# Kernel optimization log

Measured on AMD Instinct MI355X. Metric: run time of the kernel, lower is better.

Reference implementation:

```python
import jax, jax.numpy as jnp
import numpy as np

B, T, C = 2, 2048, 2048
NH, NKV, D = 16, 4, 128
N_REP = NH // NKV
THETA = 10000.0


def setup_inputs() -> dict:
    key = jax.random.key(0)
    ks = jax.random.split(key, 5)
    s = 0.02
    return {
        "x": jax.random.normal(ks[0], (B, T, C), dtype=jnp.float32),
        "Wq": jax.random.normal(ks[1], (C, C), dtype=jnp.float32) * s,
        "Wk": jax.random.normal(ks[2], (NKV * D, C), dtype=jnp.float32) * s,
        "Wv": jax.random.normal(ks[3], (NKV * D, C), dtype=jnp.float32) * s,
        "Wo": jax.random.normal(ks[4], (C, C), dtype=jnp.float32) * s,
    }


def _rope(t):
    # t: (B, H, T, D); rotate pairs (even, odd) by angle pos * theta_i
    inv_freq = 1.0 / (THETA ** (jnp.arange(0, D, 2, dtype=jnp.float32) / D))  # (D/2,)
    ang = jnp.arange(T, dtype=jnp.float32)[:, None] * inv_freq[None, :]       # (T, D/2)
    cos, sin = jnp.cos(ang), jnp.sin(ang)
    te, to = t[..., 0::2], t[..., 1::2]
    re = te * cos - to * sin
    ro = te * sin + to * cos
    return jnp.stack([re, ro], axis=-1).reshape(t.shape).astype(t.dtype)


def reference(x, Wq, Wk, Wv, Wo):
    # Projections (Linear: y = x @ W.T)
    q = (x @ Wq.T).reshape(B, T, NH, D).transpose(0, 2, 1, 3)    # (B,NH,T,D)
    k = (x @ Wk.T).reshape(B, T, NKV, D).transpose(0, 2, 1, 3)   # (B,NKV,T,D)
    v = (x @ Wv.T).reshape(B, T, NKV, D).transpose(0, 2, 1, 3)
    q = _rope(q)
    k = _rope(k)
    # GQA: group query heads per kv head instead of materializing repeated K/V
    qg = q.reshape(B, NKV, N_REP, T, D)                          # (B,G,R,T,D)
    scale = 1.0 / jnp.sqrt(jnp.float32(D))
    scores = jnp.einsum("bgrtd,bgsd->bgrts", qg, k) * scale      # (B,G,R,T,T)
    causal = jnp.tril(jnp.ones((T, T), dtype=bool))
    scores = jnp.where(causal, scores, jnp.finfo(scores.dtype).min)
    attn = jax.nn.softmax(scores, axis=-1)
    out = jnp.einsum("bgrts,bgsd->bgrtd", attn, v)               # (B,G,R,T,D)
    out = out.reshape(B, NH, T, D).transpose(0, 2, 1, 3).reshape(B, T, C)
    return out @ Wo.T
```

## Files before the change

### kernel.cpp

```cpp
#include <hip/hip_runtime.h>
#include <hip/hip_bf16.h>
#include <stdint.h>

#define B_   2
#define T_   2048
#define C_   2048
#define NH_  16
#define NKV_ 4
#define D_   128
#define NREP_ 4

typedef __attribute__((ext_vector_type(8))) short bf16x8;
typedef __attribute__((ext_vector_type(4))) float f32x4;

__device__ inline short f2bs(float f) {
    __hip_bfloat16 h = __float2bfloat16(f);
    return *reinterpret_cast<short*>(&h);
}

__device__ inline void gl_lds16(const __hip_bfloat16* g, __hip_bfloat16* l) {
    __builtin_amdgcn_global_load_lds(
        (const __attribute__((address_space(1))) unsigned int*)g,
        (__attribute__((address_space(3))) unsigned int*)l,
        16, 0, 0);
}

__global__ void prep_kernel(const float* __restrict__ x,  const float* __restrict__ Wq,
                            const float* __restrict__ Wk, const float* __restrict__ Wv,
                            const float* __restrict__ Wo,
                            __hip_bfloat16* __restrict__ xb, __hip_bfloat16* __restrict__ wcat,
                            __hip_bfloat16* __restrict__ wob, float2* __restrict__ ropeTab) {
    int tid = blockIdx.x * blockDim.x + threadIdx.x;
    const int CVT_THREADS = 4718592;
    if (tid < CVT_THREADS) {
        int i4 = tid * 4;
        const float* src;
        __hip_bfloat16* dst;
        int off;
        if (i4 < 8388608)       { src = x;  dst = xb;             off = i4; }
        else if (i4 < 12582912) { src = Wq; dst = wcat;           off = i4 - 8388608; }
        else if (i4 < 13631488) { src = Wk; dst = wcat + 4194304; off = i4 - 12582912; }
        else if (i4 < 14680064) { src = Wv; dst = wcat + 5242880; off = i4 - 13631488; }
        else                    { src = Wo; dst = wob;            off = i4 - 14680064; }
        float4 v = *reinterpret_cast<const float4*>(src + off);
        short4 o;
        o.x = f2bs(v.x); o.y = f2bs(v.y); o.z = f2bs(v.z); o.w = f2bs(v.w);
        *reinterpret_cast<short4*>(dst + off) = o;
    } else {
        int e = tid - CVT_THREADS;
        if (e < 131072) {
            int t = e >> 6, p = e & 63;
            float inv = __expf(-(float)p * (9.210340371976184f / 64.0f));
            float ang = (float)t * inv;
            ropeTab[e] = make_float2(cosf(ang), sinf(ang));
        }
    }
}

__device__ inline void storeC(float* p, float v) { *p = v; }
__device__ inline void storeC(__hip_bfloat16* p, float v) { *p = __float2bfloat16(v); }

template <typename OutT>
__global__ __launch_bounds__(256) void gemm_bt(const __hip_bfloat16* __restrict__ A,
                                               const __hip_bfloat16* __restrict__ Bm,
                                               OutT* __restrict__ Cm,
                                               int M, int N, int K) {
    __shared__ __hip_bfloat16 As[128 * 32];
    __shared__ __hip_bfloat16 Bs[128 * 32];
    const int tid  = threadIdx.x;
    const int lane = tid & 63;
    const int wv   = tid >> 6;
    const int m0 = blockIdx.y * 128, n0 = blockIdx.x * 128;
    const int wm = (wv >> 1) * 64, wn = (wv & 1) * 64;
    const int q16 = lane >> 4, r16 = lane & 15;

    f32x4 acc[4][4] = {};

    const int lrow = tid >> 2;
    const int lcol = (tid & 3) * 8;
    const __hip_bfloat16* aG = A  + (size_t)(m0 + lrow) * K + lcol;
    const __hip_bfloat16* bG = Bm + (size_t)(n0 + lrow) * K + lcol;
    __hip_bfloat16* aL = As + tid * 8;
    __hip_bfloat16* bL = Bs + tid * 8;

    for (int k0 = 0; k0 < K; k0 += 32) {
        __syncthreads();
        gl_lds16(aG + k0,          aL);
        gl_lds16(aG + 64 * K + k0, aL + 2048);
        gl_lds16(bG + k0,          bL);
        gl_lds16(bG + 64 * K + k0, bL + 2048);
        __syncthreads();
        bf16x8 af[4], bfr[4];
#pragma unroll
        for (int i = 0; i < 4; i++)
            af[i] = *reinterpret_cast<const bf16x8*>(As + (wm + i * 16 + r16) * 32 + q16 * 8);
#pragma unroll
        for (int j = 0; j < 4; j++)
            bfr[j] = *reinterpret_cast<const bf16x8*>(Bs + (wn + j * 16 + r16) * 32 + q16 * 8);
#pragma unroll
        for (int i = 0; i < 4; i++)
#pragma unroll
            for (int j = 0; j < 4; j++)
                acc[i][j] = __builtin_amdgcn_mfma_f32_16x16x32_bf16(af[i], bfr[j], acc[i][j], 0, 0, 0);
    }

#pragma unroll
    for (int i = 0; i < 4; i++)
#pragma unroll
        for (int j = 0; j < 4; j++)
#pragma unroll
            for (int r = 0; r < 4; r++) {
                int row = m0 + wm + i * 16 + q16 * 4 + r;
                int col = n0 + wn + j * 16 + r16;
                storeC(&Cm[(size_t)row * N + col], acc[i][j][r]);
            }
}

__global__ __launch_bounds__(256) void gemm_qkv(const __hip_bfloat16* __restrict__ A,
                                                const __hip_bfloat16* __restrict__ Bm,
                                                const float2* __restrict__ ropeTab,
                                                __hip_bfloat16* __restrict__ qo,
                                                __hip_bfloat16* __restrict__ ko,
                                                __hip_bfloat16* __restrict__ vT) {
    const int K = 2048;
    __shared__ __hip_bfloat16 As[128 * 32];
    __shared__ __hip_bfloat16 Bs[128 * 32];
    const int tid  = threadIdx.x;
    const int lane = tid & 63;
    const int wv   = tid >> 6;
    const int m0 = blockIdx.y * 128, n0 = blockIdx.x * 128;
    const int wm = (wv >> 1) * 64, wn = (wv & 1) * 64;
    const int q16 = lane >> 4, r16 = lane & 15;

    f32x4 acc[4][4] = {};

    const int lrow = tid >> 2;
    const int lcol = (tid & 3) * 8;
    const __hip_bfloat16* aG = A  + (size_t)(m0 + lrow) * K + lcol;
    const __hip_bfloat16* bG = Bm + (size_t)(n0 + lrow) * K + lcol;
    __hip_bfloat16* aL = As + tid * 8;
    __hip_bfloat16* bL = Bs + tid * 8;

    for (int k0 = 0; k0 < K; k0 += 32) {
        __syncthreads();
        gl_lds16(aG + k0,          aL);
        gl_lds16(aG + 64 * K + k0, aL + 2048);
        gl_lds16(bG + k0,          bL);
        gl_lds16(bG + 64 * K + k0, bL + 2048);
        __syncthreads();
        bf16x8 af[4], bfr[4];
#pragma unroll
        for (int i = 0; i < 4; i++)
            af[i] = *reinterpret_cast<const bf16x8*>(As + (wm + i * 16 + r16) * 32 + q16 * 8);
#pragma unroll
        for (int j = 0; j < 4; j++)
            bfr[j] = *reinterpret_cast<const bf16x8*>(Bs + (wn + j * 16 + r16) * 32 + q16 * 8);
#pragma unroll
        for (int i = 0; i < 4; i++)
#pragma unroll
            for (int j = 0; j < 4; j++)
                acc[i][j] = __builtin_amdgcn_mfma_f32_16x16x32_bf16(af[i], bfr[j], acc[i][j], 0, 0, 0);
    }

    const int hb = n0 >> 7;
    const float sgn = (r16 & 1) ? 1.0f : -1.0f;
#pragma unroll
    for (int i = 0; i < 4; i++)
#pragma unroll
        for (int r = 0; r < 4; r++) {
            const int m = m0 + wm + i * 16 + q16 * 4 + r;
            const int b = m >> 11, t = m & 2047;
            if (hb < 20) {
                const float2* tabRow = ropeTab + t * 64;
                __hip_bfloat16* dst = (hb < 16)
                    ? qo + ((size_t)(b * NH_ + hb) * T_ + t) * D_
                    : ko + ((size_t)(b * NKV_ + (hb - 16)) * T_ + t) * D_;
#pragma unroll
                for (int j = 0; j < 4; j++) {
                    const int dloc = wn + j * 16 + r16;
                    float v = acc[i][j][r];
                    float prt = __shfl_xor(v, 1);
                    float2 cs = tabRow[dloc >> 1];
                    float res = fmaf(prt * sgn, cs.y, v * cs.x);
                    dst[dloc] = __float2bfloat16(res);
                }
            } else {
                __hip_bfloat16* dst = vT + (size_t)(b * NKV_ + (hb - 20)) * D_ * T_ + t;
#pragma unroll
                for (int j = 0; j < 4; j++) {
                    const int d = wn + j * 16 + r16;
                    dst[(size_t)d * T_] = __float2bfloat16(acc[i][j][r]);
                }
            }
        }
}

__global__ __launch_bounds__(256, 3) void attn_kernel(const __hip_bfloat16* __restrict__ Q,
                                                      const __hip_bfloat16* __restrict__ Kt,
                                                      const __hip_bfloat16* __restrict__ Vt,
                                                      __hip_bfloat16* __restrict__ Ao,
                                                      float* __restrict__ O0,
                                                      float* __restrict__ O1,
                                                      float* __restrict__ l0p,
                                                      float* __restrict__ l1p) {
    __shared__ __hip_bfloat16 Ks[2][4096];
    __shared__ __hip_bfloat16 Vs[2][4096];
    __shared__ __hip_bfloat16 Pl[4][1280];

    const int lane = threadIdx.x & 63, wv = threadIdx.x >> 6;
    const int bg = blockIdx.y;
    const int u  = (int)blockIdx.x;
    int tb, nIt, sIdx;
    if (u < 32)      { tb = u;      nIt = tb + 1;      sIdx = -1; }
    else if (u < 64) { tb = u;      nIt = 32;          sIdx = 0;  }
    else             { tb = u - 32; nIt = tb + 1 - 32; sIdx = 1;  }
    const int sBase = (sIdx == 1) ? 1024 : 0;
    const int b = bg >> 2, g = bg & 3;
    const int h = g * 4 + wv;
    const int t0 = tb * 32;
    const int q16 = lane >> 4, r16 = lane & 15;

    const __hip_bfloat16* qh = Q + ((size_t)((b * NH_ + h) * T_) + t0) * D_;
    const __hip_bfloat16* kh = Kt + (size_t)(b * NKV_ + g) * T_ * D_;
    const __hip_bfloat16* vh = Vt + (size_t)(b * NKV_ + g) * D_ * T_;

    bf16x8 bqA[4], bqB[4];
#pragma unroll
    for (int kk = 0; kk < 4; kk++) {
        bqA[kk] = *reinterpret_cast<const bf16x8*>(qh + (size_t)r16 * D_ + kk * 32 + q16 * 8);
        bqB[kk] = *reinterpret_cast<const bf16x8*>(qh + (size_t)(16 + r16) * D_ + kk * 32 + q16 * 8);
    }

    float liA = 0.f, liB = 0.f;
    f32x4 oA[8], oB[8];
#pragma unroll
    for (int d = 0; d < 8; d++) {
        oA[d] = (f32x4){0.f, 0.f, 0.f, 0.f};
        oB[d] = (f32x4){0.f, 0.f, 0.f, 0.f};
    }

    const float SCL2 = 0.088388347648318447f * 1.4426950408889634f;
    const int tqA = t0 + r16;
    const int tqB = t0 + 16 + r16;

    const __hip_bfloat16* gK = kh + (size_t)((wv & 1) * 16 + r16) * D_ + q16 * 8;
    const __hip_bfloat16* gV = vh + (size_t)(((wv - 2) * 4) * 16 + r16) * T_ + q16 * 8;

#define STAGE(bufi, s0_)                                                        \
    do {                                                                        \
        if (wv < 2) {                                                           \
            const __hip_bfloat16* gp = gK + (size_t)(s0_) * D_;                 \
            __hip_bfloat16* lp = &Ks[bufi][(wv * 4) * 512] + lane * 8;          \
            gl_lds16(gp,      lp);                                              \
            gl_lds16(gp + 32, lp + 512);                                        \
            gl_lds16(gp + 64, lp + 1024);                                       \
            gl_lds16(gp + 96, lp + 1536);                                      \
        } else {                                                                \
            const __hip_bfloat16* gp = gV + (s0_);                              \
            __hip_bfloat16* lp = &Vs[bufi][((wv - 2) * 4) * 512] + lane * 8;    \
            gl_lds16(gp,                      lp);                              \
            gl_lds16(gp + (size_t)16 * T_,    lp + 512);                        \
            gl_lds16(gp + (size_t)32 * T_,    lp + 1024);                       \
            gl_lds16(gp + (size_t)48 * T_,    lp + 1536);                       \
        }                                                                       \
    } while (0)

    STAGE(0, sBase);

    for (int j = 0; j < nIt; j++) {
        const int s0 = sBase + j * 32;
        const int cur = j & 1;
        __syncthreads();
        if (j + 1 < nIt) STAGE(cur ^ 1, s0 + 32);

        f32x4 sc0A = (f32x4){0.f, 0.f, 0.f, 0.f};
        f32x4 sc1A = (f32x4){0.f, 0.f, 0.f, 0.f};
        f32x4 sc0B = (f32x4){0.f, 0.f, 0.f, 0.f};
        f32x4 sc1B = (f32x4){0.f, 0.f, 0.f, 0.f};
        {
            bf16x8 ak[4];
#pragma unroll
            for (int kk = 0; kk < 4; kk++)
                ak[kk] = *reinterpret_cast<const bf16x8*>(&Ks[cur][kk * 512] + lane * 8);
#pragma unroll
            for (int kk = 0; kk < 4; kk++) {
                sc0A = __builtin_amdgcn_mfma_f32_16x16x32_bf16(ak[kk], bqA[kk], sc0A, 0, 0, 0);
                sc0B = __builtin_amdgcn_mfma_f32_16x16x32_bf16(ak[kk], bqB[kk], sc0B, 0, 0, 0);
            }
#pragma unroll
            for (int kk = 0; kk < 4; kk++)
                ak[kk] = *reinterpret_cast<const bf16x8*>(&Ks[cur][(4 + kk) * 512] + lane * 8);
#pragma unroll
            for (int kk = 0; kk < 4; kk++) {
                sc1A = __builtin_amdgcn_mfma_f32_16x16x32_bf16(ak[kk], bqA[kk], sc1A, 0, 0, 0);
                sc1B = __builtin_amdgcn_mfma_f32_16x16x32_bf16(ak[kk], bqB[kk], sc1B, 0, 0, 0);
            }
        }

        ushort4 w0A, w1A, w0B, w1B;
        float psA = 0.f, psB = 0.f;
        if (s0 + 32 > t0) {
#pragma unroll
            for (int r = 0; r < 4; r++) {
                int s_a = s0 + q16 * 4 + r;
                float pa0 = (s_a <= tqA)      ? __builtin_amdgcn_exp2f(sc0A[r] * SCL2) : 0.f;
                float pa1 = (s_a + 16 <= tqA) ? __builtin_amdgcn_exp2f(sc1A[r] * SCL2) : 0.f;
                float pb0 = (s_a <= tqB)      ? __builtin_amdgcn_exp2f(sc0B[r] * SCL2) : 0.f;
                float pb1 = (s_a + 16 <= tqB) ? __builtin_amdgcn_exp2f(sc1B[r] * SCL2) : 0.f;
                psA += pa0 + pa1;
                psB += pb0 + pb1;
                ((unsigned short*)&w0A)[r] = (unsigned short)f2bs(pa0);
                ((unsigned short*)&w1A)[r] = (unsigned short)f2bs(pa1);
                ((unsigned short*)&w0B)[r] = (unsigned short)f2bs(pb0);
                ((unsigned short*)&w1B)[r] = (unsigned short)f2bs(pb1);
            }
        } else {
#pragma unroll
            for (int r = 0; r < 4; r++) {
                float pa0 = __builtin_amdgcn_exp2f(sc0A[r] * SCL2);
                float pa1 = __builtin_amdgcn_exp2f(sc1A[r] * SCL2);
                float pb0 = __builtin_amdgcn_exp2f(sc0B[r] * SCL2);
                float pb1 = __builtin_amdgcn_exp2f(sc1B[r] * SCL2);
                psA += pa0 + pa1;
                psB += pb0 + pb1;
                ((unsigned short*)&w0A)[r] = (unsigned short)f2bs(pa0);
                ((unsigned short*)&w1A)[r] = (unsigned short)f2bs(pa1);
                ((unsigned short*)&w0B)[r] = (unsigned short)f2bs(pb0);
                ((unsigned short*)&w1B)[r] = (unsigned short)f2bs(pb1);
            }
        }
        liA += psA;
        liB += psB;

        *reinterpret_cast<ushort4*>(&Pl[wv][r16 * 40 + q16 * 4]) = w0A;
        *reinterpret_cast<ushort4*>(&Pl[wv][r16 * 40 + 16 + q16 * 4]) = w1A;
        *reinterpret_cast<ushort4*>(&Pl[wv][640 + r16 * 40 + q16 * 4]) = w0B;
        *reinterpret_cast<ushort4*>(&Pl[wv][640 + r16 * 40 + 16 + q16 * 4]) = w1B;
        asm volatile("s_waitcnt lgkmcnt(0)" ::: "memory");
        bf16x8 pfA = *reinterpret_cast<const bf16x8*>(&Pl[wv][r16 * 40 + q16 * 8]);
        bf16x8 pfB = *reinterpret_cast<const bf16x8*>(&Pl[wv][640 + r16 * 40 + q16 * 8]);

#pragma unroll
        for (int d = 0; d < 8; d++) {
            bf16x8 bv = *reinterpret_cast<const bf16x8*>(&Vs[cur][d * 512] + lane * 8);
            oA[d] = __builtin_amdgcn_mfma_f32_16x16x32_bf16(pfA, bv, oA[d], 0, 0, 0);
            oB[d] = __builtin_amdgcn_mfma_f32_16x16x32_bf16(pfB, bv, oB[d], 0, 0, 0);
        }
    }

    liA += __shfl_xor(liA, 16);
    liA += __shfl_xor(liA, 32);
    liB += __shfl_xor(liB, 16);
    liB += __shfl_xor(liB, 32);

    if (sIdx < 0) {
#pragma unroll
        for (int r = 0; r < 4; r++) {
            float lrA = __shfl(liA, q16 * 4 + r, 16);
            float lrB = __shfl(liB, q16 * 4 + r, 16);
            float invA = 1.0f / lrA;
            float invB = 1.0f / lrB;
            int tA = t0 + q16 * 4 + r;
            __hip_bfloat16* dstA = Ao + (size_t)(b * T_ + tA) * C_ + h * D_ + r16;
            __hip_bfloat16* dstB = dstA + (size_t)16 * C_;
#pragma unroll
            for (int d = 0; d < 8; d++) {
                dstA[d * 16] = __float2bfloat16(oA[d][r] * invA);
                dstB[d * 16] = __float2bfloat16(oB[d][r] * invB);
            }
        }
    } else {
        float* Os = (sIdx == 0) ? O0 : O1;
        float* ls = (sIdx == 0) ? l0p : l1p;
        const size_t rb = (size_t)(b * NH_ + h) * 1024 + (size_t)(t0 - 1024);
        if (q16 == 0) {
            ls[rb + r16]      = liA;
            ls[rb + 16 + r16] = liB;
        }
#pragma unroll
        for (int r = 0; r < 4; r++) {
            int rowl = q16 * 4 + r;
            float* dA = Os + (rb + rowl) * 128 + r16;
            float* dB = Os + (rb + 16 + rowl) * 128 + r16;
#pragma unroll
            for (int d = 0; d < 8; d++) {
                dA[d * 16] = oA[d][r];
                dB[d * 16] = oB[d][r];
            }
        }
    }
#undef STAGE
}

__global__ void attn_combine(const float* __restrict__ O0, const float* __restrict__ O1,
                             const float* __restrict__ l0, const float* __restrict__ l1,
                             __hip_bfloat16* __restrict__ Ao) {
    int idx = blockIdx.x * blockDim.x + threadIdx.x;
    int row = idx >> 5, d4 = (idx & 31) << 2;
    int bh = row >> 10, tl = row & 1023;
    int b = bh >> 4, h = bh & 15;
    float inv = 1.0f / (l0[row] + l1[row]);
    float4 a = *reinterpret_cast<const float4*>(O0 + (size_t)row * 128 + d4);
    float4 c = *reinterpret_cast<const float4*>(O1 + (size_t)row * 128 + d4);
    short4 o;
    o.x = f2bs((a.x + c.x) * inv);
    o.y = f2bs((a.y + c.y) * inv);
    o.z = f2bs((a.z + c.z) * inv);
    o.w = f2bs((a.w + c.w) * inv);
    *reinterpret_cast<short4*>(Ao + (size_t)(b * T_ + 1024 + tl) * C_ + h * D_ + d4) = o;
}

extern "C" void kernel_launch(void* const* d_in, const int* in_sizes, int n_in,
                              void* d_out, int out_size, void* d_ws, size_t ws_size,
                              hipStream_t stream) {
    const float* x  = (const float*)d_in[0];
    const float* Wq = (const float*)d_in[1];
    const float* Wk = (const float*)d_in[2];
    const float* Wv = (const float*)d_in[3];
    const float* Wo = (const float*)d_in[4];
    float* out = (float*)d_out;
    char* ws = (char*)d_ws;

    __hip_bfloat16* xb   = (__hip_bfloat16*)(ws + 0);
    __hip_bfloat16* wcat = (__hip_bfloat16*)(ws + 16777216);
    float2*         ropeTab = (float2*)(ws + 29360128);
    __hip_bfloat16* wob  = (__hip_bfloat16*)(ws + 30408704);
    __hip_bfloat16* qatt = (__hip_bfloat16*)(ws + 38797312);
    __hip_bfloat16* katt = (__hip_bfloat16*)(ws + 55574528);
    __hip_bfloat16* vT   = (__hip_bfloat16*)(ws + 59768832);
    __hip_bfloat16* aout = (__hip_bfloat16*)(ws + 63963136);
    float* O0 = (float*)(ws + 0);
    float* O1 = (float*)(ws + 80740352);
    float* l0 = (float*)(ws + 97517568);
    float* l1 = (float*)(ws + 97648640);

    const int thr = 256;
    prep_kernel<<<18944, thr, 0, stream>>>(x, Wq, Wk, Wv, Wo, xb, wcat, wob, ropeTab);

    gemm_qkv<<<dim3(24, 32), 256, 0, stream>>>(xb, wcat, ropeTab, qatt, katt, vT);

    attn_kernel<<<dim3(96, 8), 256, 0, stream>>>(qatt, katt, vT, aout, O0, O1, l0, l1);
    attn_combine<<<(2 * NH_ * 1024 * 32) / thr, thr, 0, stream>>>(O0, O1, l0, l1, aout);

    gemm_bt<float><<<dim3(16, 32), 256, 0, stream>>>(aout, wob, out, 4096, 2048, 2048);
}
```

Measured before the change: 304.6 us.

## Replace 128x128 GEMMs with pipelined 256x256 swizzled-LDS GEMM kernel

Both projection GEMMs (QKV with fused RoPE and output projection) move to a single templated 256x256-tile kernel with 512 threads and 128 KB of dynamic LDS. The new kernel uses K-step 64, a double-buffered pipeline built from explicit waitcnt and barrier phases, XOR-swizzled LDS to avoid bank conflicts, s_setprio around MFMA bursts, and a block-index remap for L2 locality. The goal is more data reuse per tile and overlap of global loads with MFMA, in exchange for fewer blocks (192 and 128) on a 256-CU part, which may leave CUs idle.

Measured after the change: 306.5 us. Within noise of the previous version (+0.6%).

```diff
diff --git a/kernel.cpp b/kernel.cpp
--- a/kernel.cpp
+++ b/kernel.cpp
@@ -57,142 +57,172 @@
     }
 }
 
-__device__ inline void storeC(float* p, float v) { *p = v; }
-__device__ inline void storeC(__hip_bfloat16* p, float v) { *p = __float2bfloat16(v); }
-
-template <typename OutT>
-__global__ __launch_bounds__(256) void gemm_bt(const __hip_bfloat16* __restrict__ A,
-                                               const __hip_bfloat16* __restrict__ Bm,
-                                               OutT* __restrict__ Cm,
-                                               int M, int N, int K) {
-    __shared__ __hip_bfloat16 As[128 * 32];
-    __shared__ __hip_bfloat16 Bs[128 * 32];
-    const int tid  = threadIdx.x;
+template <int MODE, int NTN>
+__global__ __launch_bounds__(512, 2) void gemm256(
+    const __hip_bfloat16* __restrict__ A,
+    const __hip_bfloat16* __restrict__ Bm,
+    const float2* __restrict__ ropeTab,
+    __hip_bfloat16* __restrict__ qo,
+    __hip_bfloat16* __restrict__ ko,
+    __hip_bfloat16* __restrict__ vT,
+    float* __restrict__ Cout) {
+    constexpr int K = 2048;
+    constexpr int NT = K / 64;
+    extern __shared__ char lds[];
+
+    const int tid = threadIdx.x;
     const int lane = tid & 63;
-    const int wv   = tid >> 6;
-    const int m0 = blockIdx.y * 128, n0 = blockIdx.x * 128;
-    const int wm = (wv >> 1) * 64, wn = (wv & 1) * 64;
+    const int wid = tid >> 6;
+    const int wm = wid >> 2, wn = wid & 3;
     const int q16 = lane >> 4, r16 = lane & 15;
 
-    f32x4 acc[4][4] = {};
-
-    const int lrow = tid >> 2;
-    const int lcol = (tid & 3) * 8;
-    const __hip_bfloat16* aG = A  + (size_t)(m0 + lrow) * K + lcol;
-    const __hip_bfloat16* bG = Bm + (size_t)(n0 + lrow) * K + lcol;
-    __hip_bfloat16* aL = As + tid * 8;
-    __hip_bfloat16* bL = Bs + tid * 8;
-
-    for (int k0 = 0; k0 < K; k0 += 32) {
-        __syncthreads();
-        gl_lds16(aG + k0,          aL);
-        gl_lds16(aG + 64 * K + k0, aL + 2048);
-        gl_lds16(bG + k0,          bL);
-        gl_lds16(bG + 64 * K + k0, bL + 2048);
-        __syncthreads();
-        bf16x8 af[4], bfr[4];
-#pragma unroll
-        for (int i = 0; i < 4; i++)
-            af[i] = *reinterpret_cast<const bf16x8*>(As + (wm + i * 16 + r16) * 32 + q16 * 8);
-#pragma unroll
-        for (int j = 0; j < 4; j++)
-            bfr[j] = *reinterpret_cast<const bf16x8*>(Bs + (wn + j * 16 + r16) * 32 + q16 * 8);
-#pragma unroll
-        for (int i = 0; i < 4; i++)
-#pragma unroll
-            for (int j = 0; j < 4; j++)
-                acc[i][j] = __builtin_amdgcn_mfma_f32_16x16x32_bf16(af[i], bfr[j], acc[i][j], 0, 0, 0);
-    }
-
-#pragma unroll
-    for (int i = 0; i < 4; i++)
-#pragma unroll
-        for (int j = 0; j < 4; j++)
+    const int cpx = (int)gridDim.x >> 3;
+    const int bs = ((int)blockIdx.x & 7) * cpx + ((int)blockIdx.x >> 3);
+    const int tm = bs / NTN, tn = bs % NTN;
+    const int rmA = tm * 256, rmB = tn * 256;
+
+    char* const aBuf0 = lds + wm * 16384;
+    char* const aBuf1 = lds + 32768 + wm * 16384;
+    char* const bBuf0 = lds + 65536 + (wn >> 1) * 16384;
+    char* const bBuf1 = lds + 65536 + 32768 + (wn >> 1) * 16384;
+
+    const int sw  = (r16 & 7) << 4;
+    const int cS0 = (q16 << 4) ^ sw;
+    const int cS1 = (64 | (q16 << 4)) ^ sw;
+    const int rA128 = r16 * 128;
+    const int rB128 = ((wn & 1) * 64 + r16) * 128;
+
+    f32x4 acc[8][4] = {};
+    bf16x8 aF[4][2], bF[2][2][2];
+
+#define STG(Mp, rowbase, kstep, ldsoff)                                              \
+    { _Pragma("unroll") for (int li = 0; li < 2; li++) {                             \
+        const int L_ = li * 8192 + tid * 16;                                         \
+        const int rw_ = L_ >> 7;                                                     \
+        const int cb_ = (L_ & 127) ^ ((rw_ & 7) << 4);                               \
+        gl_lds16(Mp + (size_t)((rowbase) + rw_) * K + (kstep) * 64 + (cb_ >> 1),     \
+                 (__hip_bfloat16*)(lds + (ldsoff) + L_));                            \
+    } }
+#define RDA(base, a)                                                                 \
+    { _Pragma("unroll") for (int mi = 0; mi < 4; mi++) {                             \
+        const char* p_ = (base) + (a) * 8192 + mi * 2048 + rA128;                    \
+        aF[mi][0] = *(const bf16x8*)(p_ + cS0);                                      \
+        aF[mi][1] = *(const bf16x8*)(p_ + cS1);                                      \
+    } }
+#define RDB(base, b)                                                                 \
+    { _Pragma("unroll") for (int nj = 0; nj < 2; nj++) {                             \
+        const char* p_ = (base) + (b) * 4096 + nj * 2048 + rB128;                    \
+        bF[b][nj][0] = *(const bf16x8*)(p_ + cS0);                                   \
+        bF[b][nj][1] = *(const bf16x8*)(p_ + cS1);                                   \
+    } }
+#define MM(a, b)                                                                     \
+    { _Pragma("unroll") for (int mi = 0; mi < 4; mi++)                               \
+      _Pragma("unroll") for (int nj = 0; nj < 2; nj++) {                             \
+        acc[(a)*4+mi][(b)*2+nj] = __builtin_amdgcn_mfma_f32_16x16x32_bf16(           \
+            aF[mi][0], bF[(b)][nj][0], acc[(a)*4+mi][(b)*2+nj], 0, 0, 0);            \
+        acc[(a)*4+mi][(b)*2+nj] = __builtin_amdgcn_mfma_f32_16x16x32_bf16(           \
+            aF[mi][1], bF[(b)][nj][1], acc[(a)*4+mi][(b)*2+nj], 0, 0, 0);            \
+    } }
+#define BAR  __builtin_amdgcn_s_barrier()
+#define LGK0 asm volatile("s_waitcnt lgkmcnt(0)" ::: "memory")
+#define VM6  asm volatile("s_waitcnt vmcnt(6)" ::: "memory")
+#define VM0  asm volatile("s_waitcnt vmcnt(0)" ::: "memory")
+#define PRIO_MM(a, b)                                                                \
+    __builtin_amdgcn_s_setprio(1); MM(a, b); __builtin_amdgcn_s_setprio(0)
+#define STEP(AB_, BB_, S0_, S2_, S3a_, S3b_, VMW_)                                   \
+    RDA(AB_, 0); RDB(BB_, 0); S0_;                                                   \
+    BAR; LGK0; PRIO_MM(0, 0); BAR;                                                   \
+    RDB(BB_, 1);                                                                     \
+    BAR; LGK0; PRIO_MM(0, 1); BAR;                                                   \
+    RDA(AB_, 1); S2_;                                                                \
+    BAR; LGK0; PRIO_MM(1, 0); BAR;                                                   \
+    S3a_; S3b_;                                                                      \
+    BAR; LGK0; PRIO_MM(1, 1); VMW_; BAR;
+
+    STG(A,  rmA,       0, 0);
+    STG(A,  rmA + 128, 0, 16384);
+    STG(Bm, rmB,       0, 65536);
+    STG(Bm, rmB + 128, 0, 65536 + 16384);
+    STG(A,  rmA,       1, 32768);
+    STG(Bm, rmB,       1, 65536 + 32768);
+    STG(Bm, rmB + 128, 1, 65536 + 32768 + 16384);
+    VM6; BAR;
+
+    for (int u = 0; u < NT - 2; u += 2) {
+        STEP(aBuf0, bBuf0,
+             STG(A,  rmA + 128, u + 1, 32768 + 16384),
+             STG(Bm, rmB,       u + 2, 65536),
+             STG(A,  rmA,       u + 2, 0),
+             STG(Bm, rmB + 128, u + 2, 65536 + 16384),
+             VM6)
+        STEP(aBuf1, bBuf1,
+             STG(A,  rmA + 128, u + 2, 16384),
+             STG(Bm, rmB,       u + 3, 65536 + 32768),
+             STG(A,  rmA,       u + 3, 32768),
+             STG(Bm, rmB + 128, u + 3, 65536 + 32768 + 16384),
+             VM6)
+    }
+    STEP(aBuf0, bBuf0,
+         STG(A, rmA + 128, NT - 1, 32768 + 16384),
+         ((void)0), ((void)0), ((void)0),
+         VM0)
+    STEP(aBuf1, bBuf1, ((void)0), ((void)0), ((void)0), ((void)0), ((void)0))
+
+#undef STEP
+#undef PRIO_MM
+#undef VM0
+#undef VM6
+#undef LGK0
+#undef BAR
+#undef MM
+#undef RDB
+#undef RDA
+#undef STG
+
+    if constexpr (MODE == 0) {
+        constexpr int N = NTN * 256;
+        float* const cbase = Cout + (size_t)(rmA + wm * 128) * N + tn * 256 + wn * 64 + r16;
+#pragma unroll
+        for (int Ai = 0; Ai < 8; Ai++)
 #pragma unroll
             for (int r = 0; r < 4; r++) {
-                int row = m0 + wm + i * 16 + q16 * 4 + r;
-                int col = n0 + wn + j * 16 + r16;
-                storeC(&Cm[(size_t)row * N + col], acc[i][j][r]);
-            }
-}
-
-__global__ __launch_bounds__(256) void gemm_qkv(const __hip_bfloat16* __restrict__ A,
-                                                const __hip_bfloat16* __restrict__ Bm,
-                                                const float2* __restrict__ ropeTab,
-                                                __hip_bfloat16* __restrict__ qo,
-                                                __hip_bfloat16* __restrict__ ko,
-                                                __hip_bfloat16* __restrict__ vT) {
-    const int K = 2048;
-    __shared__ __hip_bfloat16 As[128 * 32];
-    __shared__ __hip_bfloat16 Bs[128 * 32];
-    const int tid  = threadIdx.x;
-    const int lane = tid & 63;
-    const int wv   = tid >> 6;
-    const int m0 = blockIdx.y * 128, n0 = blockIdx.x * 128;
-    const int wm = (wv >> 1) * 64, wn = (wv & 1) * 64;
-    const int q16 = lane >> 4, r16 = lane & 15;
-
-    f32x4 acc[4][4] = {};
-
-    const int lrow = tid >> 2;
-    const int lcol = (tid & 3) * 8;
-    const __hip_bfloat16* aG = A  + (size_t)(m0 + lrow) * K + lcol;
-    const __hip_bfloat16* bG = Bm + (size_t)(n0 + lrow) * K + lcol;
-    __hip_bfloat16* aL = As + tid * 8;
-    __hip_bfloat16* bL = Bs + tid * 8;
-
-    for (int k0 = 0; k0 < K; k0 += 32) {
-        __syncthreads();
-        gl_lds16(aG + k0,          aL);
-        gl_lds16(aG + 64 * K + k0, aL + 2048);
-        gl_lds16(bG + k0,          bL);
-        gl_lds16(bG + 64 * K + k0, bL + 2048);
-        __syncthreads();
-        bf16x8 af[4], bfr[4];
-#pragma unroll
-        for (int i = 0; i < 4; i++)
-            af[i] = *reinterpret_cast<const bf16x8*>(As + (wm + i * 16 + r16) * 32 + q16 * 8);
-#pragma unroll
-        for (int j = 0; j < 4; j++)
-            bfr[j] = *reinterpret_cast<const bf16x8*>(Bs + (wn + j * 16 + r16) * 32 + q16 * 8);
-#pragma unroll
-        for (int i = 0; i < 4; i++)
-#pragma unroll
-            for (int j = 0; j < 4; j++)
-                acc[i][j] = __builtin_amdgcn_mfma_f32_16x16x32_bf16(af[i], bfr[j], acc[i][j], 0, 0, 0);
-    }
-
-    const int hb = n0 >> 7;
-    const float sgn = (r16 & 1) ? 1.0f : -1.0f;
-#pragma unroll
-    for (int i = 0; i < 4; i++)
-#pragma unroll
-        for (int r = 0; r < 4; r++) {
-            const int m = m0 + wm + i * 16 + q16 * 4 + r;
-            const int b = m >> 11, t = m & 2047;
-            if (hb < 20) {
-                const float2* tabRow = ropeTab + t * 64;
-                __hip_bfloat16* dst = (hb < 16)
-                    ? qo + ((size_t)(b * NH_ + hb) * T_ + t) * D_
-                    : ko + ((size_t)(b * NKV_ + (hb - 16)) * T_ + t) * D_;
-#pragma unroll
-                for (int j = 0; j < 4; j++) {
-                    const int dloc = wn + j * 16 + r16;
-                    float v = acc[i][j][r];
-                    float prt = __shfl_xor(v, 1);
-                    float2 cs = tabRow[dloc >> 1];
-                    float res = fmaf(prt * sgn, cs.y, v * cs.x);
-                    dst[dloc] = __float2bfloat16(res);
+                float* dst = cbase + (size_t)(Ai * 16 + q16 * 4 + r) * N;
+#pragma unroll
+                for (int Bi = 0; Bi < 4; Bi++)
+                    dst[Bi * 16] = acc[Ai][Bi][r];
+            }
+    } else {
+        const int hb = tn * 2 + (wn >> 1);
+        const float sgn = (r16 & 1) ? 1.0f : -1.0f;
+#pragma unroll
+        for (int Ai = 0; Ai < 8; Ai++)
+#pragma unroll
+            for (int r = 0; r < 4; r++) {
+                const int m = rmA + wm * 128 + Ai * 16 + q16 * 4 + r;
+                const int bb = m >> 11, t = m & 2047;
+                if (hb < 20) {
+                    const float2* tabRow = ropeTab + t * 64;
+                    __hip_bfloat16* dst = (hb < 16)
+                        ? qo + ((size_t)(bb * NH_ + hb) * T_ + t) * D_
+                        : ko + ((size_t)(bb * NKV_ + (hb - 16)) * T_ + t) * D_;
+#pragma unroll
+                    for (int Bi = 0; Bi < 4; Bi++) {
+                        const int dloc = (wn & 1) * 64 + Bi * 16 + r16;
+                        float v = acc[Ai][Bi][r];
+                        float prt = __shfl_xor(v, 1);
+                        float2 cs = tabRow[dloc >> 1];
+                        dst[dloc] = __float2bfloat16(fmaf(prt * sgn, cs.y, v * cs.x));
+                    }
+                } else {
+                    __hip_bfloat16* dst = vT + (size_t)(bb * NKV_ + (hb - 20)) * D_ * T_ + t;
+#pragma unroll
+                    for (int Bi = 0; Bi < 4; Bi++) {
+                        const int dloc = (wn & 1) * 64 + Bi * 16 + r16;
+                        dst[(size_t)dloc * T_] = __float2bfloat16(acc[Ai][Bi][r]);
+                    }
                 }
-            } else {
-                __hip_bfloat16* dst = vT + (size_t)(b * NKV_ + (hb - 20)) * D_ * T_ + t;
-#pragma unroll
-                for (int j = 0; j < 4; j++) {
-                    const int d = wn + j * 16 + r16;
-                    dst[(size_t)d * T_] = __float2bfloat16(acc[i][j][r]);
-                }
-            }
-        }
+            }
+    }
 }
 
 __global__ __launch_bounds__(256, 3) void attn_kernel(const __hip_bfloat16* __restrict__ Q,
@@ -253,15 +283,15 @@
             __hip_bfloat16* lp = &Ks[bufi][(wv * 4) * 512] + lane * 8;          \
             gl_lds16(gp,      lp);                                              \
             gl_lds16(gp + 32, lp + 512);                                        \
-            gl_lds16(gp + 64, lp + 1024);                                       \
+            gl_lds16(gp + 64, lp + 1024);                                      \
             gl_lds16(gp + 96, lp + 1536);                                      \
         } else {                                                                \
             const __hip_bfloat16* gp = gV + (s0_);                              \
             __hip_bfloat16* lp = &Vs[bufi][((wv - 2) * 4) * 512] + lane * 8;    \
             gl_lds16(gp,                      lp);                              \
             gl_lds16(gp + (size_t)16 * T_,    lp + 512);                        \
-            gl_lds16(gp + (size_t)32 * T_,    lp + 1024);                       \
-            gl_lds16(gp + (size_t)48 * T_,    lp + 1536);                       \
+            gl_lds16(gp + (size_t)32 * T_,    lp + 1024);                      \
+            gl_lds16(gp + (size_t)48 * T_,    lp + 1536);                      \
         }                                                                       \
     } while (0)
 
@@ -434,13 +464,22 @@
     float* l0 = (float*)(ws + 97517568);
     float* l1 = (float*)(ws + 97648640);
 
+    static bool s_attr_done = false;
+    if (!s_attr_done) {
+        hipFuncSetAttribute(reinterpret_cast<const void*>(&gemm256<1, 12>),
+                            hipFuncAttributeMaxDynamicSharedMemorySize, 131072);
+        hipFuncSetAttribute(reinterpret_cast<const void*>(&gemm256<0, 8>),
+                            hipFuncAttributeMaxDynamicSharedMemorySize, 131072);
+        s_attr_done = true;
+    }
+
     const int thr = 256;
     prep_kernel<<<18944, thr, 0, stream>>>(x, Wq, Wk, Wv, Wo, xb, wcat, wob, ropeTab);
 
-    gemm_qkv<<<dim3(24, 32), 256, 0, stream>>>(xb, wcat, ropeTab, qatt, katt, vT);
+    gemm256<1, 12><<<192, 512, 131072, stream>>>(xb, wcat, ropeTab, qatt, katt, vT, nullptr);
 
     attn_kernel<<<dim3(96, 8), 256, 0, stream>>>(qatt, katt, vT, aout, O0, O1, l0, l1);
     attn_combine<<<(2 * NH_ * 1024 * 32) / thr, thr, 0, stream>>>(O0, O1, l0, l1, aout);
 
-    gemm_bt<float><<<dim3(16, 32), 256, 0, stream>>>(aout, wob, out, 4096, 2048, 2048);
-}
+    gemm256<0, 8><<<128, 512, 131072, stream>>>(aout, wob, nullptr, nullptr, nullptr, nullptr, out);
+}
```
